# Kernel tuning notes

Hardware: AMD Instinct MI355X
Metric: run time of the kernel (lower is better)

## Reference

```python
import jax, jax.numpy as jnp
import numpy as np

NUM_FEATURES = 5
MUL_FACTOR = 2.0


def setup_inputs() -> dict:
    key = jax.random.key(0)
    x = jax.random.normal(key, (4096, 512), dtype=jnp.float32)
    # buffer from __init__: mul_factor ** (arange(F) - F // 2)
    bandwidth_multipliers = (MUL_FACTOR ** (jnp.arange(NUM_FEATURES) - NUM_FEATURES // 2)).astype(jnp.float32)
    return {"x": x, "bandwidth_multipliers": bandwidth_multipliers}


def _cdist(x):
    # pairwise Euclidean distance, p=2
    sq = jnp.sum(x * x, axis=1)
    d2 = sq[:, None] + sq[None, :] - 2.0 * (x @ x.T)
    return jnp.sqrt(jnp.maximum(d2, 0.0))


def reference(x, bandwidth_multipliers):
    d = _cdist(x)  # [N, N]
    n = d.shape[0]
    # heuristic bandwidth on detached distances (self.bandwidth is None)
    bw = jax.lax.stop_gradient(d).sum() / (n * (n - 1))
    bws = bw * bandwidth_multipliers  # [F]
    # exp over F bandwidths, summed: [F, N, N] -> [N, N]
    return jnp.exp(-d[None, :, :] / bws[:, None, None]).sum(axis=0)
```

## Files before the change

### kernel.cpp

```cpp
#include <hip/hip_runtime.h>
#include <cstdint>
#include <cstddef>

#define N_PTS 4096
#define KDIM  512
#define NFEAT 5
#define NTILES 528

typedef __attribute__((ext_vector_type(8))) short bf16x8;
typedef __attribute__((ext_vector_type(4))) float f32x4;
typedef uint32_t u32;

__device__ inline unsigned short f2bf(float f) {
  union { float f; u32 u; } v; v.f = f;
  u32 r = (v.u + 0x7fffu + ((v.u >> 16) & 1u)) >> 16;
  return (unsigned short)r;
}

__device__ inline void bf2f2(u32 u, float& a, float& b) {
  union { u32 u; float f; } x, y;
  x.u = u << 16; y.u = u & 0xffff0000u;
  a = x.f; b = y.f;
}

__device__ inline void load_lds16(const void* g, void* l) {
  __builtin_amdgcn_global_load_lds(
      (const __attribute__((address_space(1))) void*)g,
      (__attribute__((address_space(3))) void*)l, 16, 0, 0);
}

__global__ __launch_bounds__(256) void prep_kernel(const float* __restrict__ X,
                                                   short* __restrict__ Xb,
                                                   float* __restrict__ sq,
                                                   float* __restrict__ gsum) {
  if (blockIdx.x == 0 && threadIdx.x == 0) *gsum = 0.f;
  const int row = blockIdx.x;
  const int t = threadIdx.x;
  const float2 v = ((const float2*)(X + (size_t)row * KDIM))[t];
  short2 b;
  b.x = (short)f2bf(v.x);
  b.y = (short)f2bf(v.y);
  ((short2*)(Xb + (size_t)row * KDIM))[t] = b;
  float s = v.x * v.x + v.y * v.y;
#pragma unroll
  for (int off = 32; off; off >>= 1) s += __shfl_down(s, off);
  __shared__ float ws[4];
  if ((t & 63) == 0) ws[t >> 6] = s;
  __syncthreads();
  if (t == 0) sq[row] = ws[0] + ws[1] + ws[2] + ws[3];
}

#define GEMM_TILE(bm, bn, acc, As, Bs)                                        \
  {                                                                           \
    const size_t ga0 = (size_t)((bm)*128 + srow) * KDIM + sgran * 8;          \
    const size_t gb0 = (size_t)((bn)*128 + srow) * KDIM + sgran * 8;          \
    for (int kt = 0; kt < KDIM / 64; ++kt) {                                  \
      const int koff = kt * 64;                                               \
      _Pragma("unroll") for (int g = 0; g < 4; ++g) {                         \
        load_lds16(Xb + ga0 + (size_t)g * 32 * KDIM + koff,                   \
                   (char*)As + g * 4096 + tid * 16);                          \
        load_lds16(Xb + gb0 + (size_t)g * 32 * KDIM + koff,                   \
                   (char*)Bs + g * 4096 + tid * 16);                          \
      }                                                                       \
      __syncthreads();                                                        \
      _Pragma("unroll") for (int h = 0; h < 2; ++h) {                         \
        bf16x8 a[4], b[4];                                                    \
        _Pragma("unroll") for (int i = 0; i < 4; ++i) {                       \
          const int ra = wave_m * 64 + i * 16 + llo;                          \
          const int rb = wave_n * 64 + i * 16 + llo;                          \
          const int c = h * 4 + lhi;                                          \
          a[i] = *(const bf16x8*)&As[ra * 64 + ((c ^ (ra & 7)) << 3)];        \
          b[i] = *(const bf16x8*)&Bs[rb * 64 + ((c ^ (rb & 7)) << 3)];        \
        }                                                                     \
        _Pragma("unroll") for (int i = 0; i < 4; ++i)                         \
            _Pragma("unroll") for (int j = 0; j < 4; ++j)                     \
                acc[i][j] = __builtin_amdgcn_mfma_f32_16x16x32_bf16(          \
                    a[i], b[j], acc[i][j], 0, 0, 0);                          \
      }                                                                       \
      __syncthreads();                                                        \
    }                                                                         \
  }

__global__ __launch_bounds__(256, 2) void dist_kernel(
    const short* __restrict__ Xb, const float* __restrict__ sq,
    unsigned short* __restrict__ Dw, float* __restrict__ gsum) {
  __shared__ short As[128 * 64];
  __shared__ short Bs[128 * 64];
  __shared__ float red[4];

  const int tid = threadIdx.x;
  const int lane = tid & 63;
  const int wid = tid >> 6;
  const int wave_m = wid >> 1, wave_n = wid & 1;
  const int lhi = lane >> 4, llo = lane & 15;
  const int srow = tid >> 3;
  const int sgran = (tid & 7) ^ (srow & 7);

  int t = (int)blockIdx.x;
  int bm = 0;
  while (t >= 32 - bm) { t -= 32 - bm; ++bm; }
  const int bn = bm + t;

  f32x4 acc[4][4];
#pragma unroll
  for (int i = 0; i < 4; ++i)
#pragma unroll
    for (int j = 0; j < 4; ++j) acc[i][j] = (f32x4){0.f, 0.f, 0.f, 0.f};

  GEMM_TILE(bm, bn, acc, As, Bs);

  float lsum = 0.f;
  const int gi0 = bm * 128, gj0 = bn * 128;
  const int r_base = wave_m * 64 + lhi * 4;
  const int c_base = wave_n * 64 + llo;
  float sqj[4];
#pragma unroll
  for (int j = 0; j < 4; ++j) sqj[j] = sq[gj0 + c_base + j * 16];

  const size_t tile_base =
      (size_t)blockIdx.x * 16384 + (size_t)wid * 4096;

#pragma unroll
  for (int i = 0; i < 4; ++i) {
    union { unsigned short s[16]; uint4 q[2]; } pk;
#pragma unroll
    for (int rr = 0; rr < 4; ++rr) {
      const int r = r_base + i * 16 + rr;
      const float sqi = sq[gi0 + r];
#pragma unroll
      for (int j = 0; j < 4; ++j) {
        const int c = c_base + j * 16;
        float d2 = sqi + sqj[j] - 2.f * acc[i][j][rr];
        float dd = sqrtf(fmaxf(d2, 0.f));
        if (gi0 + r == gj0 + c) dd = 0.f;
        lsum += dd;
        pk.s[rr * 4 + j] = f2bf(dd);
      }
    }
    unsigned short* dst = Dw + tile_base + (size_t)i * 1024;
    *(uint4*)(dst + lane * 8) = pk.q[0];
    *(uint4*)(dst + 512 + lane * 8) = pk.q[1];
  }

#pragma unroll
  for (int off = 32; off; off >>= 1) lsum += __shfl_down(lsum, off);
  if (lane == 0) red[wid] = lsum;
  __syncthreads();
  if (tid == 0) {
    const float w = (bm == bn) ? 1.f : 2.f;
    atomicAdd(gsum, w * (red[0] + red[1] + red[2] + red[3]));
  }
}

__global__ __launch_bounds__(256) void rbf_kernel(
    const unsigned short* __restrict__ Dw, const float* __restrict__ gsum,
    const float* __restrict__ mult, float* __restrict__ out) {
  __shared__ float T[32 * 132];

  const int tid = threadIdx.x;
  const int lane = tid & 63;
  const int wid = tid >> 6;
  const int wave_m = wid >> 1, wave_n = wid & 1;
  const int lhi = lane >> 4, llo = lane & 15;

  int t = (int)blockIdx.x;
  int bm = 0;
  while (t >= 32 - bm) { t -= 32 - bm; ++bm; }
  const int bn = bm + t;
  const bool diag = (bm == bn);

  const float bw = *gsum * (1.0f / ((float)N_PTS * (float)(N_PTS - 1)));
  const float m0 = mult[0], m1 = mult[1], m2 = mult[2], m3 = mult[3],
              m4 = mult[4];
  const bool fast = (m0 == 0.25f && m1 == 0.5f && m2 == 1.0f && m3 == 2.0f &&
                     m4 == 4.0f);
  const float c1 = -1.0f / (bw * m2);
  float cf[NFEAT];
  cf[0] = -1.0f / (bw * m0); cf[1] = -1.0f / (bw * m1); cf[2] = c1;
  cf[3] = -1.0f / (bw * m3); cf[4] = -1.0f / (bw * m4);

  const size_t tile_base =
      (size_t)blockIdx.x * 16384 + (size_t)wid * 4096;

  uint4 q[4][2];
#pragma unroll
  for (int i = 0; i < 4; ++i) {
    const unsigned short* src = Dw + tile_base + (size_t)i * 1024;
    q[i][0] = *(const uint4*)(src + lane * 8);
    q[i][1] = *(const uint4*)(src + 512 + lane * 8);
  }

  const int gi0 = bm * 128, gj0 = bn * 128;
  const int r_off = wave_m * 64 + lhi * 4;
  const int c_off = wave_n * 64 + llo;

#pragma unroll
  for (int i = 0; i < 4; ++i) {
    float v[16];
    bf2f2(q[i][0].x, v[0], v[1]);   bf2f2(q[i][0].y, v[2], v[3]);
    bf2f2(q[i][0].z, v[4], v[5]);   bf2f2(q[i][0].w, v[6], v[7]);
    bf2f2(q[i][1].x, v[8], v[9]);   bf2f2(q[i][1].y, v[10], v[11]);
    bf2f2(q[i][1].z, v[12], v[13]); bf2f2(q[i][1].w, v[14], v[15]);

    float o[16];
    if (fast) {
#pragma unroll
      for (int e = 0; e < 16; ++e) {
        const float tt = __expf(v[e] * c1);
        const float t2 = tt * tt;
        const float t4 = t2 * t2;
        const float s = sqrtf(tt);
        const float qq = sqrtf(s);
        o[e] = t4 + t2 + tt + s + qq;
      }
    } else {
#pragma unroll
      for (int e = 0; e < 16; ++e) {
        float a = 0.f;
#pragma unroll
        for (int f = 0; f < NFEAT; ++f) a += __expf(v[e] * cf[f]);
        o[e] = a;
      }
    }

#pragma unroll
    for (int rr = 0; rr < 4; ++rr) {
      float* orow = out + (size_t)(gi0 + r_off + i * 16 + rr) * N_PTS + gj0;
#pragma unroll
      for (int j = 0; j < 4; ++j) orow[c_off + j * 16] = o[rr * 4 + j];
    }

    if (!diag) {
#pragma unroll
      for (int rr = 0; rr < 4; ++rr)
#pragma unroll
        for (int j = 0; j < 4; ++j)
          T[(wave_m * 16 + lhi * 4 + rr) * 132 + wave_n * 64 + j * 16 + llo] =
              o[rr * 4 + j];
      __syncthreads();
      const int c = tid >> 1;
      const int g = tid & 1;
      float w[16];
#pragma unroll
      for (int k = 0; k < 16; ++k) w[k] = T[(g * 16 + k) * 132 + c];
      float* mrow =
          out + (size_t)(gj0 + c) * N_PTS + gi0 + g * 64 + i * 16;
      *(float4*)(mrow + 0) = (float4){w[0], w[1], w[2], w[3]};
      *(float4*)(mrow + 4) = (float4){w[4], w[5], w[6], w[7]};
      *(float4*)(mrow + 8) = (float4){w[8], w[9], w[10], w[11]};
      *(float4*)(mrow + 12) = (float4){w[12], w[13], w[14], w[15]};
      __syncthreads();
    }
  }
}

extern "C" void kernel_launch(void* const* d_in, const int* in_sizes, int n_in,
                              void* d_out, int out_size, void* d_ws, size_t ws_size,
                              hipStream_t stream) {
  const float* X = (const float*)d_in[0];
  const float* mult = (const float*)d_in[1];
  float* out = (float*)d_out;

  char* ws = (char*)d_ws;
  float* gsum = (float*)ws;
  float* sq = (float*)(ws + 1024);
  short* Xb = (short*)(ws + 1024 + N_PTS * sizeof(float));
  unsigned short* Dw = (unsigned short*)(ws + 1024 + N_PTS * sizeof(float) +
                                         (size_t)N_PTS * KDIM * sizeof(short));

  prep_kernel<<<N_PTS, 256, 0, stream>>>(X, Xb, sq, gsum);
  dist_kernel<<<NTILES, 256, 0, stream>>>(Xb, sq, Dw, gsum);
  rbf_kernel<<<NTILES, 256, 0, stream>>>(Dw, gsum, mult, out);
}
```

Measured before the change: 122.3 us.

## Permute B-tile rows so each lane owns 4 contiguous columns, drop LDS transpose

The B operand rows are loaded into LDS in a permuted order, so each MFMA lane's four j-accumulators map to four adjacent output columns instead of columns strided by 16. That lets the epilogue read sq with one float4 load. The rbf kernel can then write both the direct tile and the mirrored transposed tile with float4 stores straight from registers. This removes the LDS transpose buffer and its two barriers per iteration. In exchange the mirrored stores become 16-byte writes scattered across 4 rows per lane, which may coalesce less well than the previous LDS-staged row writes.

```diff
diff --git a/kernel.cpp b/kernel.cpp
--- a/kernel.cpp
+++ b/kernel.cpp
@@ -50,37 +50,6 @@
   if (t == 0) sq[row] = ws[0] + ws[1] + ws[2] + ws[3];
 }
 
-#define GEMM_TILE(bm, bn, acc, As, Bs)                                        \
-  {                                                                           \
-    const size_t ga0 = (size_t)((bm)*128 + srow) * KDIM + sgran * 8;          \
-    const size_t gb0 = (size_t)((bn)*128 + srow) * KDIM + sgran * 8;          \
-    for (int kt = 0; kt < KDIM / 64; ++kt) {                                  \
-      const int koff = kt * 64;                                               \
-      _Pragma("unroll") for (int g = 0; g < 4; ++g) {                         \
-        load_lds16(Xb + ga0 + (size_t)g * 32 * KDIM + koff,                   \
-                   (char*)As + g * 4096 + tid * 16);                          \
-        load_lds16(Xb + gb0 + (size_t)g * 32 * KDIM + koff,                   \
-                   (char*)Bs + g * 4096 + tid * 16);                          \
-      }                                                                       \
-      __syncthreads();                                                        \
-      _Pragma("unroll") for (int h = 0; h < 2; ++h) {                         \
-        bf16x8 a[4], b[4];                                                    \
-        _Pragma("unroll") for (int i = 0; i < 4; ++i) {                       \
-          const int ra = wave_m * 64 + i * 16 + llo;                          \
-          const int rb = wave_n * 64 + i * 16 + llo;                          \
-          const int c = h * 4 + lhi;                                          \
-          a[i] = *(const bf16x8*)&As[ra * 64 + ((c ^ (ra & 7)) << 3)];        \
-          b[i] = *(const bf16x8*)&Bs[rb * 64 + ((c ^ (rb & 7)) << 3)];        \
-        }                                                                     \
-        _Pragma("unroll") for (int i = 0; i < 4; ++i)                         \
-            _Pragma("unroll") for (int j = 0; j < 4; ++j)                     \
-                acc[i][j] = __builtin_amdgcn_mfma_f32_16x16x32_bf16(          \
-                    a[i], b[j], acc[i][j], 0, 0, 0);                          \
-      }                                                                       \
-      __syncthreads();                                                        \
-    }                                                                         \
-  }
-
 __global__ __launch_bounds__(256, 2) void dist_kernel(
     const short* __restrict__ Xb, const float* __restrict__ sq,
     unsigned short* __restrict__ Dw, float* __restrict__ gsum) {
@@ -107,15 +76,52 @@
 #pragma unroll
     for (int j = 0; j < 4; ++j) acc[i][j] = (f32x4){0.f, 0.f, 0.f, 0.f};
 
-  GEMM_TILE(bm, bn, acc, As, Bs);
+  const size_t ga0 = (size_t)(bm * 128 + srow) * KDIM + sgran * 8;
+  const int sB0 = 4 * (srow & 15) + (srow >> 4);
+  const size_t gb0 = (size_t)(bn * 128 + sB0) * KDIM + sgran * 8;
+  const size_t gb1 = (size_t)(bn * 128 + sB0 + 2) * KDIM + sgran * 8;
+
+  for (int kt = 0; kt < KDIM / 64; ++kt) {
+    const int koff = kt * 64;
+#pragma unroll
+    for (int g = 0; g < 4; ++g)
+      load_lds16(Xb + ga0 + (size_t)g * 32 * KDIM + koff,
+                 (char*)As + g * 4096 + tid * 16);
+    load_lds16(Xb + gb0 + koff, (char*)Bs + tid * 16);
+    load_lds16(Xb + gb1 + koff, (char*)Bs + 4096 + tid * 16);
+    load_lds16(Xb + gb0 + (size_t)64 * KDIM + koff,
+               (char*)Bs + 8192 + tid * 16);
+    load_lds16(Xb + gb1 + (size_t)64 * KDIM + koff,
+               (char*)Bs + 12288 + tid * 16);
+    __syncthreads();
+
+#pragma unroll
+    for (int h = 0; h < 2; ++h) {
+      bf16x8 a[4], b[4];
+#pragma unroll
+      for (int i = 0; i < 4; ++i) {
+        const int ra = wave_m * 64 + i * 16 + llo;
+        const int rb = wave_n * 64 + i * 16 + llo;
+        const int c = h * 4 + lhi;
+        a[i] = *(const bf16x8*)&As[ra * 64 + ((c ^ (ra & 7)) << 3)];
+        b[i] = *(const bf16x8*)&Bs[rb * 64 + ((c ^ (rb & 7)) << 3)];
+      }
+#pragma unroll
+      for (int i = 0; i < 4; ++i)
+#pragma unroll
+        for (int j = 0; j < 4; ++j)
+          acc[i][j] = __builtin_amdgcn_mfma_f32_16x16x32_bf16(
+              a[i], b[j], acc[i][j], 0, 0, 0);
+    }
+    __syncthreads();
+  }
 
   float lsum = 0.f;
   const int gi0 = bm * 128, gj0 = bn * 128;
   const int r_base = wave_m * 64 + lhi * 4;
-  const int c_base = wave_n * 64 + llo;
-  float sqj[4];
-#pragma unroll
-  for (int j = 0; j < 4; ++j) sqj[j] = sq[gj0 + c_base + j * 16];
+  const int c_base = wave_n * 64 + llo * 4;
+  const float4 sqjv = *(const float4*)(sq + gj0 + c_base);
+  const float sqj[4] = {sqjv.x, sqjv.y, sqjv.z, sqjv.w};
 
   const size_t tile_base =
       (size_t)blockIdx.x * 16384 + (size_t)wid * 4096;
@@ -129,7 +135,7 @@
       const float sqi = sq[gi0 + r];
 #pragma unroll
       for (int j = 0; j < 4; ++j) {
-        const int c = c_base + j * 16;
+        const int c = c_base + j;
         float d2 = sqi + sqj[j] - 2.f * acc[i][j][rr];
         float dd = sqrtf(fmaxf(d2, 0.f));
         if (gi0 + r == gj0 + c) dd = 0.f;
@@ -155,8 +161,6 @@
 __global__ __launch_bounds__(256) void rbf_kernel(
     const unsigned short* __restrict__ Dw, const float* __restrict__ gsum,
     const float* __restrict__ mult, float* __restrict__ out) {
-  __shared__ float T[32 * 132];
-
   const int tid = threadIdx.x;
   const int lane = tid & 63;
   const int wid = tid >> 6;
@@ -192,7 +196,7 @@
 
   const int gi0 = bm * 128, gj0 = bn * 128;
   const int r_off = wave_m * 64 + lhi * 4;
-  const int c_off = wave_n * 64 + llo;
+  const int c_off = wave_n * 64 + llo * 4;
 
 #pragma unroll
   for (int i = 0; i < 4; ++i) {
@@ -225,31 +229,19 @@
 
 #pragma unroll
     for (int rr = 0; rr < 4; ++rr) {
-      float* orow = out + (size_t)(gi0 + r_off + i * 16 + rr) * N_PTS + gj0;
-#pragma unroll
-      for (int j = 0; j < 4; ++j) orow[c_off + j * 16] = o[rr * 4 + j];
+      float* nrow = out + (size_t)(gi0 + r_off + i * 16 + rr) * N_PTS + gj0 +
+                    c_off;
+      *(float4*)nrow = (float4){o[rr * 4 + 0], o[rr * 4 + 1], o[rr * 4 + 2],
+                                o[rr * 4 + 3]};
     }
 
     if (!diag) {
 #pragma unroll
-      for (int rr = 0; rr < 4; ++rr)
-#pragma unroll
-        for (int j = 0; j < 4; ++j)
-          T[(wave_m * 16 + lhi * 4 + rr) * 132 + wave_n * 64 + j * 16 + llo] =
-              o[rr * 4 + j];
-      __syncthreads();
-      const int c = tid >> 1;
-      const int g = tid & 1;
-      float w[16];
-#pragma unroll
-      for (int k = 0; k < 16; ++k) w[k] = T[(g * 16 + k) * 132 + c];
-      float* mrow =
-          out + (size_t)(gj0 + c) * N_PTS + gi0 + g * 64 + i * 16;
-      *(float4*)(mrow + 0) = (float4){w[0], w[1], w[2], w[3]};
-      *(float4*)(mrow + 4) = (float4){w[4], w[5], w[6], w[7]};
-      *(float4*)(mrow + 8) = (float4){w[8], w[9], w[10], w[11]};
-      *(float4*)(mrow + 12) = (float4){w[12], w[13], w[14], w[15]};
-      __syncthreads();
+      for (int j = 0; j < 4; ++j) {
+        float* mrow = out + (size_t)(gj0 + c_off + j) * N_PTS + gi0 + r_off +
+                      i * 16;
+        *(float4*)mrow = (float4){o[j], o[4 + j], o[8 + j], o[12 + j]};
+      }
     }
   }
 }
```

Measured after the change: 117.8 us (median of 2 runs). 1.04x faster.
